# Kernel optimization log

Measured on AMD Instinct MI355X. Metric: run time of the kernel, lower is better.

The kernel has to match this reference:

```python
import jax, jax.numpy as jnp
import numpy as np

N, E, DIN, HID, DOUT = 50000, 800000, 128, 128, 64
NEG_SLOPE = 0.2


def setup_inputs() -> dict:
    key = jax.random.key(0)
    ks = jax.random.split(key, 16)
    x = jax.random.normal(ks[0], (N, DIN), dtype=jnp.float32)
    edge_index = jax.random.randint(ks[1], (2, E), 0, N, dtype=jnp.int64)

    def lin(k, fan_in, fan_out):
        kw, kb = jax.random.split(k)
        s = 1.0 / np.sqrt(fan_in)
        W = jax.random.uniform(kw, (fan_in, fan_out), jnp.float32, -s, s)
        b = jax.random.uniform(kb, (fan_out,), jnp.float32, -s, s)
        return W, b

    Wl, bl = lin(ks[2], DIN, DIN)   # GATv2 lin_l
    Wr, br = lin(ks[3], DIN, DIN)   # GATv2 lin_r
    att = jax.random.uniform(ks[4], (DIN,), jnp.float32, -1.0 / np.sqrt(DIN), 1.0 / np.sqrt(DIN))
    bg = jnp.zeros((DIN,), jnp.float32)  # GAT output bias
    W1, b1 = lin(ks[5], DIN, HID)   # ChebConv K=1 -> plain linear
    W2, b2 = lin(ks[6], HID, HID)
    W3, b3 = lin(ks[7], HID, DOUT)
    return {"x": x, "edge_index": edge_index, "Wl": Wl, "bl": bl, "Wr": Wr,
            "br": br, "att": att, "bg": bg, "W1": W1, "b1": b1,
            "W2": W2, "b2": b2, "W3": W3, "b3": b3}


def reference(x, edge_index, Wl, bl, Wr, br, att, bg, W1, b1, W2, b2, W3, b3):
    n = x.shape[0]
    # GATv2Conv adds self loops by default
    loop = jnp.arange(n, dtype=edge_index.dtype)
    src = jnp.concatenate([edge_index[0], loop])  # source j
    dst = jnp.concatenate([edge_index[1], loop])  # target i

    xl = x @ Wl + bl  # [N, DIN]
    xr = x @ Wr + br  # [N, DIN]

    # GATv2 edge scores: leaky_relu(x_l[j] + x_r[i]) . att
    e = jax.nn.leaky_relu(xl[src] + xr[dst], NEG_SLOPE)  # [E+N, DIN]
    a = e @ att                                          # [E+N]

    # softmax over incoming edges of each destination node
    amax = jax.ops.segment_max(a, dst, num_segments=n)
    ea = jnp.exp(a - amax[dst])
    denom = jax.ops.segment_sum(ea, dst, num_segments=n)
    alpha = ea / denom[dst]                              # [E+N]

    # aggregate messages alpha * x_l[j] at destinations
    h = jax.ops.segment_sum(alpha[:, None] * xl[src], dst, num_segments=n) + bg

    # ChebConv with K=1 reduces to a linear layer (T_0(L) = I)
    h = jax.nn.relu(h @ W1 + b1)
    h = jax.nn.relu(h @ W2 + b2)
    # dropout_rate = 0.0 -> identity
    return h @ W3 + b3
```

## Files before the change

### kernel.cpp

```cpp
#include <hip/hip_runtime.h>
#include <hip/hip_bf16.h>

#define DIN 128
#define NEG_SLOPE 0.2f
#define PTILE 2048
#define FCAP 8192
#define CVT_BLKS 289

typedef __attribute__((ext_vector_type(8))) short bf16x8;
typedef __attribute__((ext_vector_type(8))) unsigned short u16x8;
typedef __attribute__((ext_vector_type(4))) float f32x4;
typedef __attribute__((ext_vector_type(2))) float f32x2;
typedef __attribute__((ext_vector_type(4))) unsigned int u32x4;

__device__ __forceinline__ ushort f2bf(float f) {
  unsigned u = __float_as_uint(f);
  u += 0x7FFFu + ((u >> 16) & 1u);
  return (ushort)(u >> 16);
}
__device__ __forceinline__ f32x2 bfpair(unsigned u) {
  f32x2 r;
  r.x = __uint_as_float(u << 16);
  r.y = __uint_as_float(u & 0xFFFF0000u);
  return r;
}

template <int CTRL>
__device__ __forceinline__ float dppadd(float x) {
  int v = __builtin_amdgcn_update_dpp(0, __float_as_int(x), CTRL, 0xf, 0xf, true);
  return x + __int_as_float(v);
}
__device__ __forceinline__ float red16(float t) {
  t = dppadd<0xB1>(t);
  t = dppadd<0x4E>(t);
  t = dppadd<0x141>(t);
  t = dppadd<0x140>(t);
  return t;
}

__global__ __launch_bounds__(256) void cvt_hist_kernel(
    const float* __restrict__ Wl, const float* __restrict__ Wr,
    const float* __restrict__ W1, const float* __restrict__ W2,
    const float* __restrict__ W3,
    ushort* __restrict__ WlT, ushort* __restrict__ WrT,
    ushort* __restrict__ W1T, ushort* __restrict__ W2T,
    ushort* __restrict__ W3T,
    const int* __restrict__ ei, int* __restrict__ ghist, int E) {
  if (blockIdx.x < CVT_BLKS) {
    int i = blockIdx.x * 256 + threadIdx.x;
    if (i < 16384) {
      int k = i >> 7, c = i & 127; WlT[c * 128 + k] = f2bf(Wl[i]);
    } else if (i < 32768) {
      int j = i - 16384; int k = j >> 7, c = j & 127; WrT[c * 128 + k] = f2bf(Wr[j]);
    } else if (i < 49152) {
      int j = i - 32768; int k = j >> 7, c = j & 127; W1T[c * 128 + k] = f2bf(W1[j]);
    } else if (i < 65536) {
      int j = i - 49152; int k = j >> 7, c = j & 127; W2T[c * 128 + k] = f2bf(W2[j]);
    } else if (i < 73728) {
      int j = i - 65536; int k = j >> 6, c = j & 63; W3T[c * 128 + k] = f2bf(W3[j]);
    }
  } else {
    __shared__ int h[256];
    h[threadIdx.x] = 0;
    __syncthreads();
    int tile = blockIdx.x - CVT_BLKS;
    for (int e = tile * PTILE + threadIdx.x;
         e < min(E, (tile + 1) * PTILE); e += 256)
      atomicAdd(&h[ei[E + e] >> 8], 1);
    __syncthreads();
    if (h[threadIdx.x] > 0) atomicAdd(&ghist[threadIdx.x], h[threadIdx.x]);
  }
}

__global__ __launch_bounds__(256) void scan_small_kernel(
    const int* __restrict__ ghist, int* __restrict__ cum,
    int* __restrict__ cursor) {
  __shared__ int sh[256];
  int tid = threadIdx.x;
  int v = ghist[tid];
  sh[tid] = v;
  __syncthreads();
  for (int d = 1; d < 256; d <<= 1) {
    int t = (tid >= d) ? sh[tid - d] : 0;
    __syncthreads();
    sh[tid] += t;
    __syncthreads();
  }
  int exc = sh[tid] - v;
  cum[tid] = exc;
  cursor[tid] = exc;
  if (tid == 255) cum[256] = sh[255];
}

__global__ __launch_bounds__(256) void lin_partition_kernel(
    const float* __restrict__ x,
    const ushort* __restrict__ WlT, const float* __restrict__ bl,
    const ushort* __restrict__ WrT, const float* __restrict__ br,
    ushort* __restrict__ xl, ushort* __restrict__ xr, int n, int nblk_lin,
    const int* __restrict__ ei, unsigned* __restrict__ part,
    int* __restrict__ cursor, int E) {
  if ((int)blockIdx.x < nblk_lin) {
    const int tid = threadIdx.x;
    const int wv = tid >> 6, lane = tid & 63;
    const int m = lane & 15, quad = lane >> 4;
    const int colbase = (wv & 1) * 64;
    const int nodew = blockIdx.x * 32 + (wv >> 1) * 16;
    int arow = nodew + m; if (arow >= n) arow = n - 1;
    f32x4 accl[4], accr[4];
#pragma unroll
    for (int nt = 0; nt < 4; nt++) { accl[nt] = (f32x4){0,0,0,0}; accr[nt] = (f32x4){0,0,0,0}; }
#pragma unroll
    for (int kk = 0; kk < 4; kk++) {
      int k0 = kk * 32 + quad * 8;
      const float4* xp = (const float4*)(x + (long)arow * 128 + k0);
      float4 x0 = xp[0], x1 = xp[1];
      bf16x8 af;
      af[0] = (short)f2bf(x0.x); af[1] = (short)f2bf(x0.y);
      af[2] = (short)f2bf(x0.z); af[3] = (short)f2bf(x0.w);
      af[4] = (short)f2bf(x1.x); af[5] = (short)f2bf(x1.y);
      af[6] = (short)f2bf(x1.z); af[7] = (short)f2bf(x1.w);
#pragma unroll
      for (int nt = 0; nt < 4; nt++) {
        int brow = colbase + nt * 16 + m;
        bf16x8 bl8 = *(const bf16x8*)(WlT + brow * 128 + k0);
        bf16x8 br8 = *(const bf16x8*)(WrT + brow * 128 + k0);
        accl[nt] = __builtin_amdgcn_mfma_f32_16x16x32_bf16(af, bl8, accl[nt], 0, 0, 0);
        accr[nt] = __builtin_amdgcn_mfma_f32_16x16x32_bf16(af, br8, accr[nt], 0, 0, 0);
      }
    }
#pragma unroll
    for (int nt = 0; nt < 4; nt++) {
      int col = colbase + nt * 16 + m;
      float vbl = bl[col], vbr = br[col];
#pragma unroll
      for (int r = 0; r < 4; r++) {
        int node = nodew + quad * 4 + r;
        if (node < n) {
          xl[(long)node * 128 + col] = f2bf(accl[nt][r] + vbl);
          xr[(long)node * 128 + col] = f2bf(accr[nt][r] + vbr);
        }
      }
    }
  } else {
    __shared__ int hist[256], pref[256], sexcl[256], curs[256], gbase[256];
    __shared__ unsigned buf[PTILE];
    const int tid = threadIdx.x;
    const int tile0 = ((int)blockIdx.x - nblk_lin) * PTILE;
    const int tcount = min(PTILE, E - tile0);
    hist[tid] = 0;
    __syncthreads();
    unsigned pk[PTILE / 256];
    int cnt = 0;
    for (int i = tid; i < tcount; i += 256) {
      int e = tile0 + i;
      int s = ei[e], d = ei[E + e];
      unsigned p = ((unsigned)d << 16) | (unsigned)s;
      pk[cnt++] = p;
      atomicAdd(&hist[d >> 8], 1);
    }
    __syncthreads();
    int v = hist[tid];
    pref[tid] = v;
    __syncthreads();
    for (int d = 1; d < 256; d <<= 1) {
      int t = (tid >= d) ? pref[tid - d] : 0;
      __syncthreads();
      pref[tid] += t;
      __syncthreads();
    }
    int exc = pref[tid] - v;
    sexcl[tid] = exc;
    curs[tid] = exc;
    gbase[tid] = (v > 0) ? atomicAdd(&cursor[tid], v) : 0;
    __syncthreads();
    for (int j = 0; j < cnt; j++) {
      int b = pk[j] >> 24;
      int pos = atomicAdd(&curs[b], 1);
      buf[pos] = pk[j];
    }
    __syncthreads();
    for (int i = tid; i < tcount; i += 256) {
      unsigned p = buf[i];
      int b = p >> 24;
      part[gbase[b] + (i - sexcl[b])] = p;
    }
  }
}

__global__ __launch_bounds__(512) void fine_kernel(
    const unsigned* __restrict__ part, const int* __restrict__ cum,
    int* __restrict__ offsets, ushort* __restrict__ ssrc,
    int N, int E, int nbuck) {
  __shared__ int hist[256], pref[256], curs[256];
  __shared__ unsigned buf[FCAP], buf2[FCAP];
  const int tid = threadIdx.x;
  const int b = blockIdx.x;
  const int seg0 = cum[b];
  const int len = min(cum[b + 1] - seg0, FCAP);
  if (tid < 256) hist[tid] = 0;
  __syncthreads();
  for (int i = tid; i < len; i += 512) {
    unsigned p = part[seg0 + i];
    buf[i] = p;
    atomicAdd(&hist[(p >> 16) & 255], 1);
  }
  __syncthreads();
  int v = (tid < 256) ? hist[tid] : 0;
  if (tid < 256) pref[tid] = v;
  __syncthreads();
  for (int d = 1; d < 256; d <<= 1) {
    int t = (tid >= d && tid < 256) ? pref[tid - d] : 0;
    __syncthreads();
    if (tid < 256) pref[tid] += t;
    __syncthreads();
  }
  if (tid < 256) {
    int exc = pref[tid] - v;
    curs[tid] = exc;
    int node = b * 256 + tid;
    if (node < N) offsets[node] = seg0 + exc;
  }
  if (b == nbuck - 1 && tid == 0) offsets[N] = E;
  __syncthreads();
  for (int i = tid; i < len; i += 512) {
    unsigned p = buf[i];
    int pos = atomicAdd(&curs[(p >> 16) & 255], 1);
    buf2[pos] = p;
  }
  __syncthreads();
  for (int i = tid; i < len; i += 512)
    ssrc[seg0 + i] = (ushort)(buf2[i] & 0xFFFFu);
}

__global__ __launch_bounds__(256) void node_aggr_kernel(
    const ushort* __restrict__ xl, const ushort* __restrict__ xr,
    const float* __restrict__ att, const float* __restrict__ bg,
    const int* __restrict__ offsets, const ushort* __restrict__ ssrc,
    ushort* __restrict__ h, int n) {
  int wave = (int)((blockIdx.x * (long)blockDim.x + threadIdx.x) >> 6);
  int lane = threadIdx.x & 63;
  if (wave >= n) return;
  const int node = wave;
  const int eg = lane >> 4, sl = lane & 15;
  const int beg = offsets[node];
  const int end = offsets[node + 1];
  const int last = end - 1;
  const ushort* __restrict__ xls = xl + sl * 8;
  int ia0 = beg + 2 * eg;
  int sa  = (int)ssrc[min(ia0, last)];
  int sb  = (int)ssrc[min(ia0 + 1, last)];
  int sa2 = (int)ssrc[min(ia0 + 8, last)];
  int sb2 = (int)ssrc[min(ia0 + 9, last)];
  u32x4 uva = *(const u32x4*)(xls + (long)sa * 128);
  u32x4 uvb = *(const u32x4*)(xls + (long)sb * 128);

  f32x2 a06[4], a04[4], r2[4], acc2[4];
  {
    const float4* ap = (const float4*)(att + sl * 8);
    float4 a0 = ap[0], a1 = ap[1];
    f32x2 av[4] = {{a0.x, a0.y}, {a0.z, a0.w}, {a1.x, a1.y}, {a1.z, a1.w}};
#pragma unroll
    for (int jp = 0; jp < 4; jp++) {
      a06[jp] = 0.6f * av[jp];
      a04[jp] = 0.4f * av[jp];
    }
  }
  u32x4 rv = *(const u32x4*)(xr + (long)node * 128 + sl * 8);
  u32x4 lv = *(const u32x4*)(xls + (long)node * 128);
  float denom;
  {
    f32x2 t1 = {0.f, 0.f}, t2 = {0.f, 0.f};
    f32x2 l2[4];
#pragma unroll
    for (int jp = 0; jp < 4; jp++) {
      r2[jp] = bfpair(rv[jp]);
      l2[jp] = bfpair(lv[jp]);
      f32x2 v = l2[jp] + r2[jp];
      t1 += a06[jp] * v;
      t2 += a04[jp] * __builtin_elementwise_abs(v);
    }
    float t = red16(t1.x + t1.y + t2.x + t2.y);
    float es = __expf(t);
    denom = (eg == 0) ? es : 0.f;
#pragma unroll
    for (int jp = 0; jp < 4; jp++)
      acc2[jp] = (eg == 0) ? es * l2[jp] : (f32x2){0.f, 0.f};
  }
  for (int p = beg; p < end; p += 8) {
    u32x4 ca = uva, cb = uvb;
    int ia = p + 2 * eg;
    bool cva = ia < end, cvb = ia + 1 < end;
    uva = *(const u32x4*)(xls + (long)sa2 * 128);
    uvb = *(const u32x4*)(xls + (long)sb2 * 128);
    int ian = p + 16 + 2 * eg;
    sa2 = (int)ssrc[min(ian, last)];
    sb2 = (int)ssrc[min(ian + 1, last)];
    f32x2 ua2[4], ub2[4];
    f32x2 ta1 = {0.f, 0.f}, ta2 = {0.f, 0.f};
    f32x2 tb1 = {0.f, 0.f}, tb2 = {0.f, 0.f};
#pragma unroll
    for (int jp = 0; jp < 4; jp++) {
      ua2[jp] = bfpair(ca[jp]);
      ub2[jp] = bfpair(cb[jp]);
      f32x2 va2 = ua2[jp] + r2[jp];
      f32x2 vb2 = ub2[jp] + r2[jp];
      ta1 += a06[jp] * va2;
      ta2 += a04[jp] * __builtin_elementwise_abs(va2);
      tb1 += a06[jp] * vb2;
      tb2 += a04[jp] * __builtin_elementwise_abs(vb2);
    }
    float ta = red16(ta1.x + ta1.y + ta2.x + ta2.y);
    float tb = red16(tb1.x + tb1.y + tb2.x + tb2.y);
    float ea = cva ? __expf(ta) : 0.f;
    float eb = cvb ? __expf(tb) : 0.f;
    denom += ea + eb;
#pragma unroll
    for (int jp = 0; jp < 4; jp++)
      acc2[jp] += ea * ua2[jp] + eb * ub2[jp];
  }
#pragma unroll
  for (int jp = 0; jp < 4; jp++) {
    acc2[jp].x += __shfl_xor(acc2[jp].x, 16);
    acc2[jp].y += __shfl_xor(acc2[jp].y, 16);
    acc2[jp].x += __shfl_xor(acc2[jp].x, 32);
    acc2[jp].y += __shfl_xor(acc2[jp].y, 32);
  }
  denom += __shfl_xor(denom, 16);
  denom += __shfl_xor(denom, 32);
  if (eg == 0) {
    float inv = 1.0f / denom;
    const float4* bp = (const float4*)(bg + sl * 8);
    float4 g0 = bp[0], g1 = bp[1];
    f32x2 gv[4] = {{g0.x, g0.y}, {g0.z, g0.w}, {g1.x, g1.y}, {g1.z, g1.w}};
    u16x8 o;
#pragma unroll
    for (int jp = 0; jp < 4; jp++) {
      f32x2 hv = acc2[jp] * inv + gv[jp];
      o[2 * jp]     = f2bf(hv.x);
      o[2 * jp + 1] = f2bf(hv.y);
    }
    *(u16x8*)(h + (long)node * 128 + sl * 8) = o;
  }
}

#define LDSP 136
__global__ __launch_bounds__(256) void mlp_mfma_kernel(
    const ushort* __restrict__ hb,
    const ushort* __restrict__ W1T, const float* __restrict__ b1,
    const ushort* __restrict__ W2T, const float* __restrict__ b2,
    const ushort* __restrict__ W3T, const float* __restrict__ b3,
    float* __restrict__ out, int n) {
  __shared__ ushort act[32][LDSP];
  const int tid = threadIdx.x;
  const int wv = tid >> 6, lane = tid & 63;
  const int m = lane & 15, quad = lane >> 4;
  const int half = wv & 1, ng = wv >> 1;
  const int colbase = half * 64;
  const int nodew = blockIdx.x * 32 + ng * 16;
  int arow = nodew + m; if (arow >= n) arow = n - 1;
  f32x4 acc[4];
#pragma unroll
  for (int nt = 0; nt < 4; nt++) acc[nt] = (f32x4){0,0,0,0};
#pragma unroll
  for (int kk = 0; kk < 4; kk++) {
    int k0 = kk * 32 + quad * 8;
    bf16x8 af = *(const bf16x8*)(hb + (long)arow * 128 + k0);
#pragma unroll
    for (int nt = 0; nt < 4; nt++) {
      bf16x8 b8 = *(const bf16x8*)(W1T + (colbase + nt * 16 + m) * 128 + k0);
      acc[nt] = __builtin_amdgcn_mfma_f32_16x16x32_bf16(af, b8, acc[nt], 0, 0, 0);
    }
  }
#pragma unroll
  for (int nt = 0; nt < 4; nt++) {
    int col = colbase + nt * 16 + m;
    float b = b1[col];
#pragma unroll
    for (int r = 0; r < 4; r++)
      act[ng * 16 + quad * 4 + r][col] = f2bf(fmaxf(acc[nt][r] + b, 0.f));
  }
  __syncthreads();
#pragma unroll
  for (int nt = 0; nt < 4; nt++) acc[nt] = (f32x4){0,0,0,0};
#pragma unroll
  for (int kk = 0; kk < 4; kk++) {
    int k0 = kk * 32 + quad * 8;
    bf16x8 af = *(const bf16x8*)(&act[ng * 16 + m][k0]);
#pragma unroll
    for (int nt = 0; nt < 4; nt++) {
      bf16x8 b8 = *(const bf16x8*)(W2T + (colbase + nt * 16 + m) * 128 + k0);
      acc[nt] = __builtin_amdgcn_mfma_f32_16x16x32_bf16(af, b8, acc[nt], 0, 0, 0);
    }
  }
  __syncthreads();
#pragma unroll
  for (int nt = 0; nt < 4; nt++) {
    int col = colbase + nt * 16 + m;
    float b = b2[col];
#pragma unroll
    for (int r = 0; r < 4; r++)
      act[ng * 16 + quad * 4 + r][col] = f2bf(fmaxf(acc[nt][r] + b, 0.f));
  }
  __syncthreads();
  f32x4 acc3[2];
#pragma unroll
  for (int nt = 0; nt < 2; nt++) acc3[nt] = (f32x4){0,0,0,0};
#pragma unroll
  for (int kk = 0; kk < 4; kk++) {
    int k0 = kk * 32 + quad * 8;
    bf16x8 af = *(const bf16x8*)(&act[ng * 16 + m][k0]);
#pragma unroll
    for (int nt = 0; nt < 2; nt++) {
      bf16x8 b8 = *(const bf16x8*)(W3T + (half * 32 + nt * 16 + m) * 128 + k0);
      acc3[nt] = __builtin_amdgcn_mfma_f32_16x16x32_bf16(af, b8, acc3[nt], 0, 0, 0);
    }
  }
#pragma unroll
  for (int nt = 0; nt < 2; nt++) {
    int col = half * 32 + nt * 16 + m;
    float b = b3[col];
#pragma unroll
    for (int r = 0; r < 4; r++) {
      int node = nodew + quad * 4 + r;
      if (node < n) out[(long)node * 64 + col] = acc3[nt][r] + b;
    }
  }
}

extern "C" void kernel_launch(void* const* d_in, const int* in_sizes, int n_in,
                              void* d_out, int out_size, void* d_ws, size_t ws_size,
                              hipStream_t stream) {
  const float* x   = (const float*)d_in[0];
  const int*   ei  = (const int*)d_in[1];
  const float* Wl  = (const float*)d_in[2];
  const float* bl  = (const float*)d_in[3];
  const float* Wr  = (const float*)d_in[4];
  const float* br  = (const float*)d_in[5];
  const float* att = (const float*)d_in[6];
  const float* bg  = (const float*)d_in[7];
  const float* W1  = (const float*)d_in[8];
  const float* b1  = (const float*)d_in[9];
  const float* W2  = (const float*)d_in[10];
  const float* b2  = (const float*)d_in[11];
  const float* W3  = (const float*)d_in[12];
  const float* b3  = (const float*)d_in[13];
  float* out = (float*)d_out;

  const int N = in_sizes[0] / DIN;
  const int E = in_sizes[1] / 2;
  const int nbuck = (N + 255) >> 8;

  char* ws = (char*)d_ws;
  size_t off = 0;
  auto alloc = [&](size_t bytes) {
    void* p = ws + off;
    off += (bytes + 255) & ~(size_t)255;
    return p;
  };
  int* ghist     = (int*)alloc(256 * 4);
  int* cum       = (int*)alloc(257 * 4);
  int* cursor    = (int*)alloc(256 * 4);
  int* offsets   = (int*)alloc(((size_t)N + 4) * 4);
  unsigned* part = (unsigned*)alloc((size_t)E * 4);
  ushort* ssrc   = (ushort*)alloc(((size_t)E + 16) * 2);
  ushort* xlb    = (ushort*)alloc((size_t)N * DIN * 2);
  ushort* xrb    = (ushort*)alloc((size_t)N * DIN * 2);
  ushort* hbf    = (ushort*)alloc((size_t)N * DIN * 2);
  ushort* WlT    = (ushort*)alloc(16384 * 2);
  ushort* WrT    = (ushort*)alloc(16384 * 2);
  ushort* W1T    = (ushort*)alloc(16384 * 2);
  ushort* W2T    = (ushort*)alloc(16384 * 2);
  ushort* W3T    = (ushort*)alloc(8192 * 2);
  (void)ws_size;

  hipMemsetAsync(ghist, 0, 256 * 4, stream);

  int ntile = (E + PTILE - 1) / PTILE;
  cvt_hist_kernel<<<CVT_BLKS + ntile, 256, 0, stream>>>(
      Wl, Wr, W1, W2, W3, WlT, WrT, W1T, W2T, W3T, ei, ghist, E);

  scan_small_kernel<<<1, 256, 0, stream>>>(ghist, cum, cursor);

  int nblk32 = (N + 31) / 32;
  lin_partition_kernel<<<nblk32 + ntile, 256, 0, stream>>>(
      x, WlT, bl, WrT, br, xlb, xrb, N, nblk32, ei, part, cursor, E);

  fine_kernel<<<nbuck, 512, 0, stream>>>(part, cum, offsets, ssrc, N, E, nbuck);

  int nwblk = (N + 3) / 4;
  node_aggr_kernel<<<nwblk, 256, 0, stream>>>(xlb, xrb, att, bg,
                                              offsets, ssrc, hbf, N);

  mlp_mfma_kernel<<<nblk32, 256, 0, stream>>>(hbf, W1T, b1, W2T, b2,
                                              W3T, b3, out, N);
}
```

Measured before the change: 243.4 us.

## Fuse GAT aggregation into MLP kernel and fold bucket scan into consumers

```diff
diff --git a/kernel.cpp b/kernel.cpp
--- a/kernel.cpp
+++ b/kernel.cpp
@@ -3,7 +3,7 @@
 
 #define DIN 128
 #define NEG_SLOPE 0.2f
-#define PTILE 2048
+#define PTILE 1024
 #define FCAP 8192
 #define CVT_BLKS 289
 
@@ -72,33 +72,13 @@
   }
 }
 
-__global__ __launch_bounds__(256) void scan_small_kernel(
-    const int* __restrict__ ghist, int* __restrict__ cum,
-    int* __restrict__ cursor) {
-  __shared__ int sh[256];
-  int tid = threadIdx.x;
-  int v = ghist[tid];
-  sh[tid] = v;
-  __syncthreads();
-  for (int d = 1; d < 256; d <<= 1) {
-    int t = (tid >= d) ? sh[tid - d] : 0;
-    __syncthreads();
-    sh[tid] += t;
-    __syncthreads();
-  }
-  int exc = sh[tid] - v;
-  cum[tid] = exc;
-  cursor[tid] = exc;
-  if (tid == 255) cum[256] = sh[255];
-}
-
 __global__ __launch_bounds__(256) void lin_partition_kernel(
     const float* __restrict__ x,
     const ushort* __restrict__ WlT, const float* __restrict__ bl,
     const ushort* __restrict__ WrT, const float* __restrict__ br,
     ushort* __restrict__ xl, ushort* __restrict__ xr, int n, int nblk_lin,
     const int* __restrict__ ei, unsigned* __restrict__ part,
-    int* __restrict__ cursor, int E) {
+    const int* __restrict__ ghist, int* __restrict__ cursor0, int E) {
   if ((int)blockIdx.x < nblk_lin) {
     const int tid = threadIdx.x;
     const int wv = tid >> 6, lane = tid & 63;
@@ -142,13 +122,16 @@
       }
     }
   } else {
-    __shared__ int hist[256], pref[256], sexcl[256], curs[256], gbase[256];
+    __shared__ int hist[256], pref[256], sexcl[256], curs[256], gbase[256],
+                   gsc[256];
+    const int tid = threadIdx.x;
+    const int gv0 = ghist[tid];
+    gsc[tid] = gv0;
+    hist[tid] = 0;
+    __syncthreads();
     __shared__ unsigned buf[PTILE];
-    const int tid = threadIdx.x;
     const int tile0 = ((int)blockIdx.x - nblk_lin) * PTILE;
     const int tcount = min(PTILE, E - tile0);
-    hist[tid] = 0;
-    __syncthreads();
     unsigned pk[PTILE / 256];
     int cnt = 0;
     for (int i = tid; i < tcount; i += 256) {
@@ -163,15 +146,17 @@
     pref[tid] = v;
     __syncthreads();
     for (int d = 1; d < 256; d <<= 1) {
-      int t = (tid >= d) ? pref[tid - d] : 0;
+      int t1 = (tid >= d) ? pref[tid - d] : 0;
+      int t2 = (tid >= d) ? gsc[tid - d] : 0;
       __syncthreads();
-      pref[tid] += t;
+      pref[tid] += t1;
+      gsc[tid] += t2;
       __syncthreads();
     }
     int exc = pref[tid] - v;
     sexcl[tid] = exc;
     curs[tid] = exc;
-    gbase[tid] = (v > 0) ? atomicAdd(&cursor[tid], v) : 0;
+    gbase[tid] = (gsc[tid] - gv0) + ((v > 0) ? atomicAdd(&cursor0[tid], v) : 0);
     __syncthreads();
     for (int j = 0; j < cnt; j++) {
       int b = pk[j] >> 24;
@@ -188,17 +173,26 @@
 }
 
 __global__ __launch_bounds__(512) void fine_kernel(
-    const unsigned* __restrict__ part, const int* __restrict__ cum,
+    const unsigned* __restrict__ part, const int* __restrict__ ghist,
     int* __restrict__ offsets, ushort* __restrict__ ssrc,
     int N, int E, int nbuck) {
-  __shared__ int hist[256], pref[256], curs[256];
+  __shared__ int hist[256], pref[256], curs[256], gsc[256];
   __shared__ unsigned buf[FCAP], buf2[FCAP];
   const int tid = threadIdx.x;
   const int b = blockIdx.x;
-  const int seg0 = cum[b];
-  const int len = min(cum[b + 1] - seg0, FCAP);
-  if (tid < 256) hist[tid] = 0;
-  __syncthreads();
+  if (tid < 256) {
+    gsc[tid] = ghist[tid];
+    hist[tid] = 0;
+  }
+  __syncthreads();
+  for (int d = 1; d < 256; d <<= 1) {
+    int t = (tid >= d && tid < 256) ? gsc[tid - d] : 0;
+    __syncthreads();
+    if (tid < 256) gsc[tid] += t;
+    __syncthreads();
+  }
+  const int seg0 = (b == 0) ? 0 : gsc[b - 1];
+  const int len = min(gsc[b] - seg0, FCAP);
   for (int i = tid; i < len; i += 512) {
     unsigned p = part[seg0 + i];
     buf[i] = p;
@@ -232,139 +226,138 @@
     ssrc[seg0 + i] = (ushort)(buf2[i] & 0xFFFFu);
 }
 
-__global__ __launch_bounds__(256) void node_aggr_kernel(
+#define LDSP 136
+__global__ __launch_bounds__(256) void node_mlp_kernel(
     const ushort* __restrict__ xl, const ushort* __restrict__ xr,
     const float* __restrict__ att, const float* __restrict__ bg,
     const int* __restrict__ offsets, const ushort* __restrict__ ssrc,
-    ushort* __restrict__ h, int n) {
-  int wave = (int)((blockIdx.x * (long)blockDim.x + threadIdx.x) >> 6);
-  int lane = threadIdx.x & 63;
-  if (wave >= n) return;
-  const int node = wave;
-  const int eg = lane >> 4, sl = lane & 15;
-  const int beg = offsets[node];
-  const int end = offsets[node + 1];
-  const int last = end - 1;
-  const ushort* __restrict__ xls = xl + sl * 8;
-  int ia0 = beg + 2 * eg;
-  int sa  = (int)ssrc[min(ia0, last)];
-  int sb  = (int)ssrc[min(ia0 + 1, last)];
-  int sa2 = (int)ssrc[min(ia0 + 8, last)];
-  int sb2 = (int)ssrc[min(ia0 + 9, last)];
-  u32x4 uva = *(const u32x4*)(xls + (long)sa * 128);
-  u32x4 uvb = *(const u32x4*)(xls + (long)sb * 128);
-
-  f32x2 a06[4], a04[4], r2[4], acc2[4];
-  {
-    const float4* ap = (const float4*)(att + sl * 8);
-    float4 a0 = ap[0], a1 = ap[1];
-    f32x2 av[4] = {{a0.x, a0.y}, {a0.z, a0.w}, {a1.x, a1.y}, {a1.z, a1.w}};
-#pragma unroll
-    for (int jp = 0; jp < 4; jp++) {
-      a06[jp] = 0.6f * av[jp];
-      a04[jp] = 0.4f * av[jp];
-    }
-  }
-  u32x4 rv = *(const u32x4*)(xr + (long)node * 128 + sl * 8);
-  u32x4 lv = *(const u32x4*)(xls + (long)node * 128);
-  float denom;
-  {
-    f32x2 t1 = {0.f, 0.f}, t2 = {0.f, 0.f};
-    f32x2 l2[4];
-#pragma unroll
-    for (int jp = 0; jp < 4; jp++) {
-      r2[jp] = bfpair(rv[jp]);
-      l2[jp] = bfpair(lv[jp]);
-      f32x2 v = l2[jp] + r2[jp];
-      t1 += a06[jp] * v;
-      t2 += a04[jp] * __builtin_elementwise_abs(v);
-    }
-    float t = red16(t1.x + t1.y + t2.x + t2.y);
-    float es = __expf(t);
-    denom = (eg == 0) ? es : 0.f;
-#pragma unroll
-    for (int jp = 0; jp < 4; jp++)
-      acc2[jp] = (eg == 0) ? es * l2[jp] : (f32x2){0.f, 0.f};
-  }
-  for (int p = beg; p < end; p += 8) {
-    u32x4 ca = uva, cb = uvb;
-    int ia = p + 2 * eg;
-    bool cva = ia < end, cvb = ia + 1 < end;
-    uva = *(const u32x4*)(xls + (long)sa2 * 128);
-    uvb = *(const u32x4*)(xls + (long)sb2 * 128);
-    int ian = p + 16 + 2 * eg;
-    sa2 = (int)ssrc[min(ian, last)];
-    sb2 = (int)ssrc[min(ian + 1, last)];
-    f32x2 ua2[4], ub2[4];
-    f32x2 ta1 = {0.f, 0.f}, ta2 = {0.f, 0.f};
-    f32x2 tb1 = {0.f, 0.f}, tb2 = {0.f, 0.f};
-#pragma unroll
-    for (int jp = 0; jp < 4; jp++) {
-      ua2[jp] = bfpair(ca[jp]);
-      ub2[jp] = bfpair(cb[jp]);
-      f32x2 va2 = ua2[jp] + r2[jp];
-      f32x2 vb2 = ub2[jp] + r2[jp];
-      ta1 += a06[jp] * va2;
-      ta2 += a04[jp] * __builtin_elementwise_abs(va2);
-      tb1 += a06[jp] * vb2;
-      tb2 += a04[jp] * __builtin_elementwise_abs(vb2);
-    }
-    float ta = red16(ta1.x + ta1.y + ta2.x + ta2.y);
-    float tb = red16(tb1.x + tb1.y + tb2.x + tb2.y);
-    float ea = cva ? __expf(ta) : 0.f;
-    float eb = cvb ? __expf(tb) : 0.f;
-    denom += ea + eb;
-#pragma unroll
-    for (int jp = 0; jp < 4; jp++)
-      acc2[jp] += ea * ua2[jp] + eb * ub2[jp];
-  }
-#pragma unroll
-  for (int jp = 0; jp < 4; jp++) {
-    acc2[jp].x += __shfl_xor(acc2[jp].x, 16);
-    acc2[jp].y += __shfl_xor(acc2[jp].y, 16);
-    acc2[jp].x += __shfl_xor(acc2[jp].x, 32);
-    acc2[jp].y += __shfl_xor(acc2[jp].y, 32);
-  }
-  denom += __shfl_xor(denom, 16);
-  denom += __shfl_xor(denom, 32);
-  if (eg == 0) {
-    float inv = 1.0f / denom;
-    const float4* bp = (const float4*)(bg + sl * 8);
-    float4 g0 = bp[0], g1 = bp[1];
-    f32x2 gv[4] = {{g0.x, g0.y}, {g0.z, g0.w}, {g1.x, g1.y}, {g1.z, g1.w}};
-    u16x8 o;
-#pragma unroll
-    for (int jp = 0; jp < 4; jp++) {
-      f32x2 hv = acc2[jp] * inv + gv[jp];
-      o[2 * jp]     = f2bf(hv.x);
-      o[2 * jp + 1] = f2bf(hv.y);
-    }
-    *(u16x8*)(h + (long)node * 128 + sl * 8) = o;
-  }
-}
-
-#define LDSP 136
-__global__ __launch_bounds__(256) void mlp_mfma_kernel(
-    const ushort* __restrict__ hb,
     const ushort* __restrict__ W1T, const float* __restrict__ b1,
     const ushort* __restrict__ W2T, const float* __restrict__ b2,
     const ushort* __restrict__ W3T, const float* __restrict__ b3,
     float* __restrict__ out, int n) {
+  __shared__ ushort hst[32][LDSP];
   __shared__ ushort act[32][LDSP];
   const int tid = threadIdx.x;
   const int wv = tid >> 6, lane = tid & 63;
+  {
+    const int eg = lane >> 4, sl = lane & 15;
+    const ushort* __restrict__ xls = xl + sl * 8;
+    f32x2 a06[4], a04[4], gvb[4];
+    {
+      const float4* ap = (const float4*)(att + sl * 8);
+      float4 a0 = ap[0], a1 = ap[1];
+      f32x2 av[4] = {{a0.x, a0.y}, {a0.z, a0.w}, {a1.x, a1.y}, {a1.z, a1.w}};
+#pragma unroll
+      for (int jp = 0; jp < 4; jp++) {
+        a06[jp] = 0.6f * av[jp];
+        a04[jp] = 0.4f * av[jp];
+      }
+      const float4* bp = (const float4*)(bg + sl * 8);
+      float4 g0 = bp[0], g1 = bp[1];
+      gvb[0] = (f32x2){g0.x, g0.y}; gvb[1] = (f32x2){g0.z, g0.w};
+      gvb[2] = (f32x2){g1.x, g1.y}; gvb[3] = (f32x2){g1.z, g1.w};
+    }
+    for (int nn = 0; nn < 8; nn++) {
+      const int node = (int)blockIdx.x * 32 + wv * 8 + nn;
+      if (node >= n) continue;
+      const int beg = offsets[node];
+      const int end = offsets[node + 1];
+      const int last = end - 1;
+      int ia0 = beg + 2 * eg;
+      int sa  = (int)ssrc[min(ia0, last)];
+      int sb  = (int)ssrc[min(ia0 + 1, last)];
+      int sa2 = (int)ssrc[min(ia0 + 8, last)];
+      int sb2 = (int)ssrc[min(ia0 + 9, last)];
+      u32x4 uva = *(const u32x4*)(xls + (long)sa * 128);
+      u32x4 uvb = *(const u32x4*)(xls + (long)sb * 128);
+      f32x2 r2[4], acc2[4];
+      u32x4 rv = *(const u32x4*)(xr + (long)node * 128 + sl * 8);
+      u32x4 lv = *(const u32x4*)(xls + (long)node * 128);
+      float denom;
+      {
+        f32x2 t1 = {0.f, 0.f}, t2 = {0.f, 0.f};
+        f32x2 l2[4];
+#pragma unroll
+        for (int jp = 0; jp < 4; jp++) {
+          r2[jp] = bfpair(rv[jp]);
+          l2[jp] = bfpair(lv[jp]);
+          f32x2 v = l2[jp] + r2[jp];
+          t1 += a06[jp] * v;
+          t2 += a04[jp] * __builtin_elementwise_abs(v);
+        }
+        float t = red16(t1.x + t1.y + t2.x + t2.y);
+        float es = __expf(t);
+        denom = (eg == 0) ? es : 0.f;
+#pragma unroll
+        for (int jp = 0; jp < 4; jp++)
+          acc2[jp] = (eg == 0) ? es * l2[jp] : (f32x2){0.f, 0.f};
+      }
+      for (int p = beg; p < end; p += 8) {
+        u32x4 ca = uva, cb = uvb;
+        int ia = p + 2 * eg;
+        bool cva = ia < end, cvb = ia + 1 < end;
+        uva = *(const u32x4*)(xls + (long)sa2 * 128);
+        uvb = *(const u32x4*)(xls + (long)sb2 * 128);
+        int ian = p + 16 + 2 * eg;
+        sa2 = (int)ssrc[min(ian, last)];
+        sb2 = (int)ssrc[min(ian + 1, last)];
+        f32x2 ua2[4], ub2[4];
+        f32x2 ta1 = {0.f, 0.f}, ta2 = {0.f, 0.f};
+        f32x2 tb1 = {0.f, 0.f}, tb2 = {0.f, 0.f};
+#pragma unroll
+        for (int jp = 0; jp < 4; jp++) {
+          ua2[jp] = bfpair(ca[jp]);
+          ub2[jp] = bfpair(cb[jp]);
+          f32x2 va2 = ua2[jp] + r2[jp];
+          f32x2 vb2 = ub2[jp] + r2[jp];
+          ta1 += a06[jp] * va2;
+          ta2 += a04[jp] * __builtin_elementwise_abs(va2);
+          tb1 += a06[jp] * vb2;
+          tb2 += a04[jp] * __builtin_elementwise_abs(vb2);
+        }
+        float ta = red16(ta1.x + ta1.y + ta2.x + ta2.y);
+        float tb = red16(tb1.x + tb1.y + tb2.x + tb2.y);
+        float ea = cva ? __expf(ta) : 0.f;
+        float eb = cvb ? __expf(tb) : 0.f;
+        denom += ea + eb;
+#pragma unroll
+        for (int jp = 0; jp < 4; jp++)
+          acc2[jp] += ea * ua2[jp] + eb * ub2[jp];
+      }
+#pragma unroll
+      for (int jp = 0; jp < 4; jp++) {
+        acc2[jp].x += __shfl_xor(acc2[jp].x, 16);
+        acc2[jp].y += __shfl_xor(acc2[jp].y, 16);
+        acc2[jp].x += __shfl_xor(acc2[jp].x, 32);
+        acc2[jp].y += __shfl_xor(acc2[jp].y, 32);
+      }
+      denom += __shfl_xor(denom, 16);
+      denom += __shfl_xor(denom, 32);
+      if (eg == 0) {
+        float inv = 1.0f / denom;
+        u16x8 o;
+#pragma unroll
+        for (int jp = 0; jp < 4; jp++) {
+          f32x2 hv = acc2[jp] * inv + gvb[jp];
+          o[2 * jp]     = f2bf(hv.x);
+          o[2 * jp + 1] = f2bf(hv.y);
+        }
+        *(u16x8*)(&hst[wv * 8 + nn][sl * 8]) = o;
+      }
+    }
+  }
+  __syncthreads();
   const int m = lane & 15, quad = lane >> 4;
   const int half = wv & 1, ng = wv >> 1;
   const int colbase = half * 64;
-  const int nodew = blockIdx.x * 32 + ng * 16;
-  int arow = nodew + m; if (arow >= n) arow = n - 1;
+  const int nodew = (int)blockIdx.x * 32 + ng * 16;
   f32x4 acc[4];
 #pragma unroll
   for (int nt = 0; nt < 4; nt++) acc[nt] = (f32x4){0,0,0,0};
 #pragma unroll
   for (int kk = 0; kk < 4; kk++) {
     int k0 = kk * 32 + quad * 8;
-    bf16x8 af = *(const bf16x8*)(hb + (long)arow * 128 + k0);
+    bf16x8 af = *(const bf16x8*)(&hst[ng * 16 + m][k0]);
 #pragma unroll
     for (int nt = 0; nt < 4; nt++) {
       bf16x8 b8 = *(const bf16x8*)(W1T + (colbase + nt * 16 + m) * 128 + k0);
@@ -458,14 +451,12 @@
     return p;
   };
   int* ghist     = (int*)alloc(256 * 4);
-  int* cum       = (int*)alloc(257 * 4);
-  int* cursor    = (int*)alloc(256 * 4);
+  int* cursor0   = (int*)alloc(256 * 4);
   int* offsets   = (int*)alloc(((size_t)N + 4) * 4);
   unsigned* part = (unsigned*)alloc((size_t)E * 4);
   ushort* ssrc   = (ushort*)alloc(((size_t)E + 16) * 2);
   ushort* xlb    = (ushort*)alloc((size_t)N * DIN * 2);
   ushort* xrb    = (ushort*)alloc((size_t)N * DIN * 2);
-  ushort* hbf    = (ushort*)alloc((size_t)N * DIN * 2);
   ushort* WlT    = (ushort*)alloc(16384 * 2);
   ushort* WrT    = (ushort*)alloc(16384 * 2);
   ushort* W1T    = (ushort*)alloc(16384 * 2);
@@ -473,24 +464,19 @@
   ushort* W3T    = (ushort*)alloc(8192 * 2);
   (void)ws_size;
 
-  hipMemsetAsync(ghist, 0, 256 * 4, stream);
+  hipMemsetAsync(ghist, 0, 512 * 4, stream);
 
   int ntile = (E + PTILE - 1) / PTILE;
   cvt_hist_kernel<<<CVT_BLKS + ntile, 256, 0, stream>>>(
       Wl, Wr, W1, W2, W3, WlT, WrT, W1T, W2T, W3T, ei, ghist, E);
 
-  scan_small_kernel<<<1, 256, 0, stream>>>(ghist, cum, cursor);
-
   int nblk32 = (N + 31) / 32;
   lin_partition_kernel<<<nblk32 + ntile, 256, 0, stream>>>(
-      x, WlT, bl, WrT, br, xlb, xrb, N, nblk32, ei, part, cursor, E);
-
-  fine_kernel<<<nbuck, 512, 0, stream>>>(part, cum, offsets, ssrc, N, E, nbuck);
-
-  int nwblk = (N + 3) / 4;
-  node_aggr_kernel<<<nwblk, 256, 0, stream>>>(xlb, xrb, att, bg,
-                                              offsets, ssrc, hbf, N);
-
-  mlp_mfma_kernel<<<nblk32, 256, 0, stream>>>(hbf, W1T, b1, W2T, b2,
-                                              W3T, b3, out, N);
-}
+      x, WlT, bl, WrT, br, xlb, xrb, N, nblk32, ei, part, ghist, cursor0, E);
+
+  fine_kernel<<<nbuck, 512, 0, stream>>>(part, ghist, offsets, ssrc, N, E, nbuck);
+
+  node_mlp_kernel<<<nblk32, 256, 0, stream>>>(
+      xlb, xrb, att, bg, offsets, ssrc,
+      W1T, b1, W2T, b2, W3T, b3, out, N);
+}
```

After: 253.8 us. +4.3%, slower.
